# Performance work log

Hardware: AMD Instinct MI355X
Metric: run time of the kernel (lower is better)

The kernel has to match this reference:

```python
import jax, jax.numpy as jnp
import numpy as np

B, IN, OUT = 512, 1024, 1024

def setup_inputs() -> dict:
    key = jax.random.key(0)
    kx, kw = jax.random.split(key)
    X = jax.random.normal(kx, (B, IN), dtype=jnp.float32)
    W = jax.random.normal(kw, (OUT, IN), dtype=jnp.float32) * 0.02  # init_std=0.02
    return {"X": X, "W": W}

def reference(X, W):
    # Tropical (max-plus) matmul: Y[b, j] = max_i (X[b, i] + W[j, i]).
    # leaky_factor=1 / is_random=False -> plain hard max in forward.
    # [B, 1, IN] + [1, OUT, IN] -> max over IN -> [B, OUT]
    return jnp.max(X[:, None, :] + W[None, :, :], axis=-1)
```

## Files before the change

kernel.cpp:

```cpp
#include <hip/hip_runtime.h>
#include <stdint.h>


#define M_DIM 512
#define N_DIM 1024
#define K_DIM 1024
#define CAP 128

#define OFF_WT    0
#define OFF_TMAX  (4u * 1024u * 1024u)
#define OFF_TMIN  (OFF_TMAX + 1024u)
#define OFF_XMAX  (OFF_TMIN + 1024u)

__global__ __launch_bounds__(256)
void prep(const float* __restrict__ W, const float* __restrict__ X,
          float* __restrict__ Wt, float* __restrict__ tmax,
          float* __restrict__ tmin, float* __restrict__ Xmax) {
    __shared__ float L[64][65];
    __shared__ float smx[4][64];
    __shared__ float smn[4][64];

    const int tid = threadIdx.x;
    const int bx = blockIdx.x;

    if (bx >= 256) {
        const int b = bx - 256;
        const float4 xv = ((const float4*)X)[b * (K_DIM / 4) + tid];
        float m = fmaxf(fmaxf(xv.x, xv.y), fmaxf(xv.z, xv.w));
#pragma unroll
        for (int off = 32; off > 0; off >>= 1)
            m = fmaxf(m, __shfl_down(m, off, 64));
        if ((tid & 63) == 0) smx[0][tid >> 6] = m;
        __syncthreads();
        if (tid == 0)
            Xmax[b] = fmaxf(fmaxf(smx[0][0], smx[0][1]),
                            fmaxf(smx[0][2], smx[0][3]));
        return;
    }

    const int kt = bx & 15;
    const int jt = bx >> 4;
    const int k0 = kt * 64, j0 = jt * 64;

    {
        const int r = tid >> 2, q = tid & 3;
        const float* g = &W[(size_t)(j0 + r) * K_DIM + k0 + q * 16];
#pragma unroll
        for (int t = 0; t < 4; t++) {
            float4 f = *(const float4*)(g + 4 * t);
            L[r][q * 16 + 4 * t + 0] = f.x;
            L[r][q * 16 + 4 * t + 1] = f.y;
            L[r][q * 16 + 4 * t + 2] = f.z;
            L[r][q * 16 + 4 * t + 3] = f.w;
        }
    }
    __syncthreads();
    {
        const int kk = tid >> 2, q = tid & 3;
        float* o = &Wt[(size_t)(k0 + kk) * N_DIM + j0 + q * 16];
#pragma unroll
        for (int t = 0; t < 4; t++) {
            float4 f = {L[q * 16 + 4 * t + 0][kk], L[q * 16 + 4 * t + 1][kk],
                        L[q * 16 + 4 * t + 2][kk], L[q * 16 + 4 * t + 3][kk]};
            *(float4*)(o + 4 * t) = f;
        }
    }
    {
        const int jl = tid & 63, seg = tid >> 6;
        float mx = -3.0e38f, mn = 3.0e38f;
#pragma unroll
        for (int i = 0; i < 16; i++) {
            float v = L[jl][seg * 16 + i];
            mx = fmaxf(mx, v);
            mn = fminf(mn, v);
        }
        smx[seg][jl] = mx;
        smn[seg][jl] = mn;
    }
    __syncthreads();
    if (tid < 64) {
        float mx = fmaxf(fmaxf(smx[0][tid], smx[1][tid]), fmaxf(smx[2][tid], smx[3][tid]));
        float mn = fminf(fminf(smn[0][tid], smn[1][tid]), fminf(smn[2][tid], smn[3][tid]));
#pragma unroll
        for (int off = 32; off > 0; off >>= 1) {
            mx = fmaxf(mx, __shfl_down(mx, off, 64));
            mn = fminf(mn, __shfl_down(mn, off, 64));
        }
        if (tid == 0) {
            const int id = jt * 16 + kt;
            tmax[id] = mx;
            tmin[id] = mn;
        }
    }
}

__global__ __launch_bounds__(256)
void emit_pruned(const float* __restrict__ X, const float* __restrict__ Wt,
                 const float* __restrict__ tmax, const float* __restrict__ tmin,
                 const float* __restrict__ Xmax, float* __restrict__ out) {
    __shared__ float sD;
    __shared__ float sval[CAP];
    __shared__ int sidx[CAP];
    __shared__ int scnt;

    const int tid = threadIdx.x;
    const int b = blockIdx.x;

    if (tid < 64) {
        float4 a = ((const float4*)tmax)[tid];
        float4 i = ((const float4*)tmin)[tid];
        float mx = fmaxf(fmaxf(a.x, a.y), fmaxf(a.z, a.w));
        float mn = fminf(fminf(i.x, i.y), fminf(i.z, i.w));
#pragma unroll
        for (int off = 32; off > 0; off >>= 1) {
            mx = fmaxf(mx, __shfl_down(mx, off, 64));
            mn = fminf(mn, __shfl_down(mn, off, 64));
        }
        if (tid == 0) sD = (mx - mn) * 1.0001f + 1e-6f;
    }
    if (tid == 0) scnt = 0;
    __syncthreads();
    const float thr = Xmax[b] - sD;

    const float4 xv = ((const float4*)X)[b * (K_DIM / 4) + tid];
    const float xa[4] = {xv.x, xv.y, xv.z, xv.w};
#pragma unroll
    for (int c = 0; c < 4; c++) {
        if (xa[c] > thr) {
            int p = atomicAdd(&scnt, 1);
            if (p < CAP) { sidx[p] = tid * 4 + c; sval[p] = xa[c]; }
        }
    }
    __syncthreads();
    const int n = scnt;

    float4 acc = {-3.0e38f, -3.0e38f, -3.0e38f, -3.0e38f};
    if (n <= CAP) {
        for (int c = 0; c < n; c++) {
            const int k = sidx[c];
            const float xk = sval[c];
            const float4 w = ((const float4*)Wt)[k * (N_DIM / 4) + tid];
            acc.x = fmaxf(acc.x, xk + w.x);
            acc.y = fmaxf(acc.y, xk + w.y);
            acc.z = fmaxf(acc.z, xk + w.z);
            acc.w = fmaxf(acc.w, xk + w.w);
        }
    } else {
        for (int k = 0; k < K_DIM; k++) {
            const float xk = X[(size_t)b * K_DIM + k];
            const float4 w = ((const float4*)Wt)[k * (N_DIM / 4) + tid];
            acc.x = fmaxf(acc.x, xk + w.x);
            acc.y = fmaxf(acc.y, xk + w.y);
            acc.z = fmaxf(acc.z, xk + w.z);
            acc.w = fmaxf(acc.w, xk + w.w);
        }
    }
    ((float4*)out)[b * (N_DIM / 4) + tid] = acc;
}

extern "C" void kernel_launch(void* const* d_in, const int* in_sizes, int n_in,
                              void* d_out, int out_size, void* d_ws, size_t ws_size,
                              hipStream_t stream) {
    const float* X = (const float*)d_in[0];
    const float* W = (const float*)d_in[1];
    float* out = (float*)d_out;

    char* ws = (char*)d_ws;
    float* Wt   = (float*)(ws + OFF_WT);
    float* tmax = (float*)(ws + OFF_TMAX);
    float* tmin = (float*)(ws + OFF_TMIN);
    float* Xmax = (float*)(ws + OFF_XMAX);

    prep<<<768, 256, 0, stream>>>(W, X, Wt, tmax, tmin, Xmax);
    emit_pruned<<<M_DIM, 256, 0, stream>>>(X, Wt, tmax, tmin, Xmax, out);
}
```

Baseline: 63.43 us.

## Drop W transpose; read W columns directly and compute X max inline

```diff
diff --git a/kernel.cpp b/kernel.cpp
--- a/kernel.cpp
+++ b/kernel.cpp
@@ -5,103 +5,51 @@
 #define M_DIM 512
 #define N_DIM 1024
 #define K_DIM 1024
-#define CAP 128
+#define CAP   256
+#define NSTAT 256
 
-#define OFF_WT    0
-#define OFF_TMAX  (4u * 1024u * 1024u)
-#define OFF_TMIN  (OFF_TMAX + 1024u)
-#define OFF_XMAX  (OFF_TMIN + 1024u)
+#define OFF_TMAX 0
+#define OFF_TMIN 1024u
 
 __global__ __launch_bounds__(256)
-void prep(const float* __restrict__ W, const float* __restrict__ X,
-          float* __restrict__ Wt, float* __restrict__ tmax,
-          float* __restrict__ tmin, float* __restrict__ Xmax) {
-    __shared__ float L[64][65];
-    __shared__ float smx[4][64];
-    __shared__ float smn[4][64];
-
+void wstats(const float* __restrict__ W, float* __restrict__ tmax,
+            float* __restrict__ tmin) {
+    __shared__ float smx[4];
+    __shared__ float smn[4];
     const int tid = threadIdx.x;
     const int bx = blockIdx.x;
+    const float4* W4 = (const float4*)W;
 
-    if (bx >= 256) {
-        const int b = bx - 256;
-        const float4 xv = ((const float4*)X)[b * (K_DIM / 4) + tid];
-        float m = fmaxf(fmaxf(xv.x, xv.y), fmaxf(xv.z, xv.w));
+    float mx = -3.0e38f, mn = 3.0e38f;
 #pragma unroll
-        for (int off = 32; off > 0; off >>= 1)
-            m = fmaxf(m, __shfl_down(m, off, 64));
-        if ((tid & 63) == 0) smx[0][tid >> 6] = m;
-        __syncthreads();
-        if (tid == 0)
-            Xmax[b] = fmaxf(fmaxf(smx[0][0], smx[0][1]),
-                            fmaxf(smx[0][2], smx[0][3]));
-        return;
+    for (int t = 0; t < 4; t++) {
+        float4 f = W4[(size_t)bx * 1024 + t * 256 + tid];
+        mx = fmaxf(mx, fmaxf(fmaxf(f.x, f.y), fmaxf(f.z, f.w)));
+        mn = fminf(mn, fminf(fminf(f.x, f.y), fminf(f.z, f.w)));
     }
-
-    const int kt = bx & 15;
-    const int jt = bx >> 4;
-    const int k0 = kt * 64, j0 = jt * 64;
-
-    {
-        const int r = tid >> 2, q = tid & 3;
-        const float* g = &W[(size_t)(j0 + r) * K_DIM + k0 + q * 16];
 #pragma unroll
-        for (int t = 0; t < 4; t++) {
-            float4 f = *(const float4*)(g + 4 * t);
-            L[r][q * 16 + 4 * t + 0] = f.x;
-            L[r][q * 16 + 4 * t + 1] = f.y;
-            L[r][q * 16 + 4 * t + 2] = f.z;
-            L[r][q * 16 + 4 * t + 3] = f.w;
-        }
+    for (int off = 32; off > 0; off >>= 1) {
+        mx = fmaxf(mx, __shfl_down(mx, off, 64));
+        mn = fminf(mn, __shfl_down(mn, off, 64));
     }
+    if ((tid & 63) == 0) { smx[tid >> 6] = mx; smn[tid >> 6] = mn; }
     __syncthreads();
-    {
-        const int kk = tid >> 2, q = tid & 3;
-        float* o = &Wt[(size_t)(k0 + kk) * N_DIM + j0 + q * 16];
-#pragma unroll
-        for (int t = 0; t < 4; t++) {
-            float4 f = {L[q * 16 + 4 * t + 0][kk], L[q * 16 + 4 * t + 1][kk],
-                        L[q * 16 + 4 * t + 2][kk], L[q * 16 + 4 * t + 3][kk]};
-            *(float4*)(o + 4 * t) = f;
-        }
-    }
-    {
-        const int jl = tid & 63, seg = tid >> 6;
-        float mx = -3.0e38f, mn = 3.0e38f;
-#pragma unroll
-        for (int i = 0; i < 16; i++) {
-            float v = L[jl][seg * 16 + i];
-            mx = fmaxf(mx, v);
-            mn = fminf(mn, v);
-        }
-        smx[seg][jl] = mx;
-        smn[seg][jl] = mn;
-    }
-    __syncthreads();
-    if (tid < 64) {
-        float mx = fmaxf(fmaxf(smx[0][tid], smx[1][tid]), fmaxf(smx[2][tid], smx[3][tid]));
-        float mn = fminf(fminf(smn[0][tid], smn[1][tid]), fminf(smn[2][tid], smn[3][tid]));
-#pragma unroll
-        for (int off = 32; off > 0; off >>= 1) {
-            mx = fmaxf(mx, __shfl_down(mx, off, 64));
-            mn = fminf(mn, __shfl_down(mn, off, 64));
-        }
-        if (tid == 0) {
-            const int id = jt * 16 + kt;
-            tmax[id] = mx;
-            tmin[id] = mn;
-        }
+    if (tid == 0) {
+        tmax[bx] = fmaxf(fmaxf(smx[0], smx[1]), fmaxf(smx[2], smx[3]));
+        tmin[bx] = fminf(fminf(smn[0], smn[1]), fminf(smn[2], smn[3]));
     }
 }
 
 __global__ __launch_bounds__(256)
-void emit_pruned(const float* __restrict__ X, const float* __restrict__ Wt,
+void emit_pruned(const float* __restrict__ X, const float* __restrict__ W,
                  const float* __restrict__ tmax, const float* __restrict__ tmin,
-                 const float* __restrict__ Xmax, float* __restrict__ out) {
+                 float* __restrict__ out) {
     __shared__ float sD;
+    __shared__ float sXm[4];
+    __shared__ float sX[K_DIM];
     __shared__ float sval[CAP];
-    __shared__ int sidx[CAP];
-    __shared__ int scnt;
+    __shared__ int   sidx[CAP];
+    __shared__ int   scnt;
 
     const int tid = threadIdx.x;
     const int b = blockIdx.x;
@@ -119,10 +67,19 @@
         if (tid == 0) sD = (mx - mn) * 1.0001f + 1e-6f;
     }
     if (tid == 0) scnt = 0;
-    __syncthreads();
-    const float thr = Xmax[b] - sD;
 
     const float4 xv = ((const float4*)X)[b * (K_DIM / 4) + tid];
+    *(float4*)&sX[tid * 4] = xv;
+    float m = fmaxf(fmaxf(xv.x, xv.y), fmaxf(xv.z, xv.w));
+#pragma unroll
+    for (int off = 32; off > 0; off >>= 1)
+        m = fmaxf(m, __shfl_down(m, off, 64));
+    if ((tid & 63) == 0) sXm[tid >> 6] = m;
+    __syncthreads();
+
+    const float xm = fmaxf(fmaxf(sXm[0], sXm[1]), fmaxf(sXm[2], sXm[3]));
+    const float thr = xm - sD;
+
     const float xa[4] = {xv.x, xv.y, xv.z, xv.w};
 #pragma unroll
     for (int c = 0; c < 4; c++) {
@@ -135,25 +92,33 @@
     const int n = scnt;
 
     float4 acc = {-3.0e38f, -3.0e38f, -3.0e38f, -3.0e38f};
+    const int j0 = tid * 4;
     if (n <= CAP) {
         for (int c = 0; c < n; c++) {
             const int k = sidx[c];
             const float xk = sval[c];
-            const float4 w = ((const float4*)Wt)[k * (N_DIM / 4) + tid];
-            acc.x = fmaxf(acc.x, xk + w.x);
-            acc.y = fmaxf(acc.y, xk + w.y);
-            acc.z = fmaxf(acc.z, xk + w.z);
-            acc.w = fmaxf(acc.w, xk + w.w);
+            const float* col = W + k;
+            acc.x = fmaxf(acc.x, xk + col[(size_t)(j0 + 0) * K_DIM]);
+            acc.y = fmaxf(acc.y, xk + col[(size_t)(j0 + 1) * K_DIM]);
+            acc.z = fmaxf(acc.z, xk + col[(size_t)(j0 + 2) * K_DIM]);
+            acc.w = fmaxf(acc.w, xk + col[(size_t)(j0 + 3) * K_DIM]);
         }
     } else {
-        for (int k = 0; k < K_DIM; k++) {
-            const float xk = X[(size_t)b * K_DIM + k];
-            const float4 w = ((const float4*)Wt)[k * (N_DIM / 4) + tid];
-            acc.x = fmaxf(acc.x, xk + w.x);
-            acc.y = fmaxf(acc.y, xk + w.y);
-            acc.z = fmaxf(acc.z, xk + w.z);
-            acc.w = fmaxf(acc.w, xk + w.w);
+        float ar[4];
+#pragma unroll
+        for (int r = 0; r < 4; r++) {
+            const float4* row = (const float4*)(W + (size_t)(j0 + r) * K_DIM);
+            float a = -3.0e38f;
+            for (int k4 = 0; k4 < K_DIM / 4; k4++) {
+                float4 w = row[k4];
+                a = fmaxf(a, fmaxf(fmaxf(sX[k4 * 4 + 0] + w.x,
+                                         sX[k4 * 4 + 1] + w.y),
+                                   fmaxf(sX[k4 * 4 + 2] + w.z,
+                                         sX[k4 * 4 + 3] + w.w)));
+            }
+            ar[r] = a;
         }
+        acc = make_float4(ar[0], ar[1], ar[2], ar[3]);
     }
     ((float4*)out)[b * (N_DIM / 4) + tid] = acc;
 }
@@ -166,11 +131,9 @@
     float* out = (float*)d_out;
 
     char* ws = (char*)d_ws;
-    float* Wt   = (float*)(ws + OFF_WT);
     float* tmax = (float*)(ws + OFF_TMAX);
     float* tmin = (float*)(ws + OFF_TMIN);
-    float* Xmax = (float*)(ws + OFF_XMAX);
 
-    prep<<<768, 256, 0, stream>>>(W, X, Wt, tmax, tmin, Xmax);
-    emit_pruned<<<M_DIM, 256, 0, stream>>>(X, Wt, tmax, tmin, Xmax, out);
+    wstats<<<NSTAT, 256, 0, stream>>>(W, tmax, tmin);
+    emit_pruned<<<M_DIM, 256, 0, stream>>>(X, W, tmax, tmin, out);
 }
```

After: 71.81 us. 1.13x slower.
